# Kernel tuning notes

Measured on AMD Instinct MI355X. Metric: run time of the kernel, lower is better.

Reference implementation:

```python
import jax, jax.numpy as jnp
import numpy as np

N_QUBITS = 16
DIM = 1 << N_QUBITS
NUM_CLASSES = 23
BATCH = 64

# PauliZ sign table: wire 0 is the most-significant bit of the flattened index.
_idx = np.arange(DIM)
SIGNS = np.stack([1 - 2 * ((_idx >> (N_QUBITS - 1 - w)) & 1) for w in range(N_QUBITS)], axis=1).astype(np.float32)  # (DIM, 16)


def _rx_mat(theta):
    c = jnp.cos(theta / 2).astype(jnp.complex64)
    s = (-1j * jnp.sin(theta / 2)).astype(jnp.complex64)
    return jnp.stack([jnp.stack([c, s]), jnp.stack([s, c])])  # (2,2)


def _rot_mat(phi, theta, omega):
    ct = jnp.cos(theta / 2)
    st = jnp.sin(theta / 2)
    a = jnp.exp(-0.5j * (phi + omega)) * ct
    b = -jnp.exp(0.5j * (phi - omega)) * st
    c = jnp.exp(-0.5j * (phi - omega)) * st
    d = jnp.exp(0.5j * (phi + omega)) * ct
    return jnp.stack([jnp.stack([a, b]), jnp.stack([c, d])]).astype(jnp.complex64)


def _apply_1q(state, U, w):
    # state: (B, 2,...,2); shared 2x2 gate on wire w (axis w+1)
    st = jnp.tensordot(state, U, axes=[[w + 1], [1]])  # contracted axis moves to last
    return jnp.moveaxis(st, -1, w + 1)


def _apply_rx_batched(state, theta_b, w):
    # per-sample RX angles theta_b: (B,)
    half = theta_b / 2
    c = jnp.cos(half).astype(jnp.complex64)
    s = (-1j * jnp.sin(half)).astype(jnp.complex64)
    U = jnp.stack([jnp.stack([c, s], -1), jnp.stack([s, c], -1)], -2)  # (B,2,2)
    st = jnp.moveaxis(state, w + 1, -1)
    st = jnp.einsum('bji,b...i->b...j', U, st)
    return jnp.moveaxis(st, -1, w + 1)


def _apply_crx(state, theta, ctrl, tgt):
    s0 = jax.lax.index_in_dim(state, 0, axis=ctrl + 1, keepdims=False)
    s1 = jax.lax.index_in_dim(state, 1, axis=ctrl + 1, keepdims=False)
    tax = tgt + 1 if tgt < ctrl else tgt  # target axis after control axis removal
    U = _rx_mat(theta)
    s1 = jnp.moveaxis(jnp.tensordot(s1, U, axes=[[tax], [1]]), -1, tax)
    return jnp.stack([s0, s1], axis=ctrl + 1)


def _circuit(x, w0, x0, w1, x1):
    B = x.shape[0]
    state = jnp.zeros((B,) + (2,) * N_QUBITS, jnp.complex64)
    state = state.at[(slice(None),) + (0,) * N_QUBITS].set(1.0)
    for w, xc in ((w0, x0), (w1, x1)):
        for q in range(N_QUBITS):
            state = _apply_rx_batched(state, x[:, q], q)
        for q in range(N_QUBITS):
            state = _apply_1q(state, _rot_mat(w[q, 0], w[q, 1], w[q, 2]), q)
        for q in range(N_QUBITS):
            state = _apply_crx(state, xc[q], q, (q + 1) % N_QUBITS)
    probs = (state.real ** 2 + state.imag ** 2).reshape(B, DIM)
    return probs @ jnp.asarray(SIGNS)  # (B, 16) PauliZ expvals


def setup_inputs() -> dict:
    key = jax.random.key(0)
    ks = jax.random.split(key, 7)
    return {
        'x': jax.random.normal(ks[0], (BATCH, N_QUBITS), jnp.float32),
        'w0': jax.random.normal(ks[1], (N_QUBITS, 3), jnp.float32),
        'x0': jax.random.normal(ks[2], (N_QUBITS,), jnp.float32),
        'w1': jax.random.normal(ks[3], (N_QUBITS, 3), jnp.float32),
        'x1': jax.random.normal(ks[4], (N_QUBITS,), jnp.float32),
        'fc_w': jax.random.normal(ks[5], (NUM_CLASSES, N_QUBITS), jnp.float32) * 0.25,
        'fc_b': jax.random.normal(ks[6], (NUM_CLASSES,), jnp.float32) * 0.05,
    }


def reference(x, w0, x0, w1, x1, fc_w, fc_b):
    feats = _circuit(x, w0, x0, w1, x1)           # (B, 16)
    logits = feats @ fc_w.T + fc_b                # (B, 23)
    return jax.nn.log_softmax(logits, axis=1)
```

## Files before the change

kernel.cpp:

```cpp
#include <hip/hip_runtime.h>
#include <hip/hip_bf16.h>


#define DIM 65536
#define BATCH 64
#define PSTR 580


template<int RB>
__device__ __forceinline__ void g1q_reg(float* sr, float* si, const float* U) {
  float u00r=U[0],u00i=U[1],u01r=U[2],u01i=U[3],u10r=U[4],u10i=U[5],u11r=U[6],u11i=U[7];
#pragma unroll
  for (int k = 0; k < 8; ++k) {
    int lo = k & ((1<<RB)-1);
    int j0 = ((k >> RB) << (RB+1)) | lo;
    int j1 = j0 | (1<<RB);
    float a0r=sr[j0], a0i=si[j0], a1r=sr[j1], a1i=si[j1];
    sr[j0] = u00r*a0r - u00i*a0i + u01r*a1r - u01i*a1i;
    si[j0] = u00r*a0i + u00i*a0r + u01r*a1i + u01i*a1r;
    sr[j1] = u10r*a0r - u10i*a0i + u11r*a1r - u11i*a1i;
    si[j1] = u10r*a0i + u10i*a0r + u11r*a1i + u11i*a1r;
  }
}

template<int RB, int CB>
__device__ __forceinline__ void gsel_reg_cc(float* sr, float* si, const float* M0, const float* M1) {
  float a0=M0[0],a1=M0[1],a2=M0[2],a3=M0[3],a4=M0[4],a5=M0[5],a6=M0[6],a7=M0[7];
  float b0=M1[0],b1=M1[1],b2=M1[2],b3=M1[3],b4=M1[4],b5=M1[5],b6=M1[6],b7=M1[7];
#pragma unroll
  for (int k = 0; k < 8; ++k) {
    int lo = k & ((1<<RB)-1);
    int j0 = ((k >> RB) << (RB+1)) | lo;
    int j1 = j0 | (1<<RB);
    const bool c = ((j0 >> CB) & 1) != 0;
    float u00r=c?b0:a0, u00i=c?b1:a1, u01r=c?b2:a2, u01i=c?b3:a3;
    float u10r=c?b4:a4, u10i=c?b5:a5, u11r=c?b6:a6, u11i=c?b7:a7;
    float p0r=sr[j0], p0i=si[j0], p1r=sr[j1], p1i=si[j1];
    sr[j0] = u00r*p0r - u00i*p0i + u01r*p1r - u01i*p1i;
    si[j0] = u00r*p0i + u00i*p0r + u01r*p1i + u01i*p1r;
    sr[j1] = u10r*p0r - u10i*p0i + u11r*p1r - u11i*p1i;
    si[j1] = u10r*p0i + u10i*p0r + u11r*p1i + u11i*p1r;
  }
}

template<int RB>
__device__ __forceinline__ void gsel_reg_pred(float* sr, float* si, const float* M0,
                                              const float* M1, bool ctrl) {
  float u[8];
#pragma unroll
  for (int e = 0; e < 8; ++e) u[e] = ctrl ? M1[e] : M0[e];
  g1q_reg<RB>(sr, si, u);
}

template<int CB, int LB>
__device__ __forceinline__ void crx_reg_lane(float* sr, float* si, float c, float s) {
#pragma unroll
  for (int k = 0; k < 8; ++k) {
    int lo2 = k & ((1<<CB)-1);
    int j = ((((k >> CB) << (CB+1)) | lo2)) | (1<<CB);
    float pr = __shfl_xor(sr[j], 1<<LB, 64);
    float pi = __shfl_xor(si[j], 1<<LB, 64);
    float mr = sr[j], mi = si[j];
    sr[j] = c*mr + s*pi;
    si[j] = c*mi - s*pr;
  }
}

__device__ __forceinline__ int swz(int o) { return o ^ ((o>>4)&15) ^ ((o>>8)&15); }

__device__ __forceinline__ unsigned bfp(float r, float i) {
  unsigned ur = __float_as_uint(r), ui = __float_as_uint(i);
  ur = (ur + 0x7fffu + ((ur >> 16) & 1u)) >> 16;
  ui = (ui + 0x7fffu + ((ui >> 16) & 1u)) & 0xffff0000u;
  return (ur & 0xffffu) | ui;
}
__device__ __forceinline__ float bfr(unsigned u) { return __uint_as_float(u << 16); }
__device__ __forceinline__ float bfi(unsigned u) { return __uint_as_float(u & 0xffff0000u); }

#define MP(Pb, l, q, s) ((Pb) + (((l)*16+(q))*2+(s))*8)


__global__ __launch_bounds__(256) void pB2(unsigned* __restrict__ st,
                                           const float* __restrict__ x, const float* __restrict__ w0,
                                           const float* __restrict__ x0, const float* __restrict__ w1,
                                           const float* __restrict__ x1, float* __restrict__ P,
                                           float* __restrict__ feats, int* __restrict__ ctr) {
  __shared__ float2 lds2[4096];
  __shared__ float Ps[PSTR];
  int blk = blockIdx.x;
  int b = blk >> 4, mp = blk & 15;
  int t = threadIdx.x, lane = t & 63, wv = t >> 6;

  {
    float (*su)[8] = reinterpret_cast<float(*)[8]>(lds2);
    if (mp == 0 && t < 16) feats[b*16 + t] = 0.f;
    if (mp == 0 && t == 16) ctr[b] = 0;
    if (t < 32) {
      int l = t >> 4, q = t & 15;
      const float* W = (l ? w1 : w0) + q*3;
      float xa = 0.5f * x[b*16 + q];
      float cr = cosf(xa), sx = sinf(xa);
      float phi = W[0], th = W[1], om = W[2];
      float ct = cosf(0.5f*th), stt = sinf(0.5f*th);
      float po = 0.5f*(phi+om), pm = 0.5f*(phi-om);
      float ar =  cosf(po)*ct,  ai = -sinf(po)*ct;
      float br = -cosf(pm)*stt, bi = -sinf(pm)*stt;
      float cr2 = cosf(pm)*stt, ci2 = -sinf(pm)*stt;
      float dr =  cosf(po)*ct,  di =  sinf(po)*ct;
      float U[8];
      U[0] = ar*cr + bi*sx;   U[1] = ai*cr - br*sx;
      U[2] = ai*sx + br*cr;   U[3] = -ar*sx + bi*cr;
      U[4] = cr2*cr + di*sx;  U[5] = ci2*cr - dr*sx;
      U[6] = ci2*sx + dr*cr;  U[7] = -cr2*sx + di*cr;
      float* M0 = MP(Ps, l, q, 0);
      float* M1 = M0 + 8;
#pragma unroll
      for (int e = 0; e < 8; ++e) { M0[e] = U[e]; su[t][e] = U[e]; }
      if (q == 0) {
        float ang = l ? 0.5f*x0[15] : 0.f;
        float cg = cosf(ang), sg = sinf(ang);
        M1[0] =  cg*U[0] + sg*U[3];  M1[1] = cg*U[1] - sg*U[2];
        M1[2] =  sg*U[1] + cg*U[2];  M1[3] = -sg*U[0] + cg*U[3];
        M1[4] =  cg*U[4] + sg*U[7];  M1[5] = cg*U[5] - sg*U[6];
        M1[6] =  sg*U[5] + cg*U[6];  M1[7] = -sg*U[4] + cg*U[7];
      } else {
        float ang = 0.5f*(l ? x1[q-1] : x0[q-1]);
        float cg = cosf(ang), sg = sinf(ang);
        M1[0] = cg*U[0] + sg*U[5];  M1[1] = cg*U[1] - sg*U[4];
        M1[2] = cg*U[2] + sg*U[7];  M1[3] = cg*U[3] - sg*U[6];
        M1[4] = cg*U[4] + sg*U[1];  M1[5] = cg*U[5] - sg*U[0];
        M1[6] = cg*U[6] + sg*U[3];  M1[7] = cg*U[7] - sg*U[2];
      }
      if (t == 0) { Ps[576] = cosf(0.5f*x1[15]); Ps[577] = sinf(0.5f*x1[15]); }
    }
    __syncthreads();
  }

  float sr[16], si[16];
#pragma unroll
  for (int r = 0; r < 16; ++r) { sr[r] = 0.f; si[r] = 0.f; }
  if (t == 0) {
    sr[0] = 1.f;
    g1q_reg<3>(sr, si, MP(Ps,0,0,0));
    gsel_reg_cc<2,3>(sr, si, MP(Ps,0,1,0), MP(Ps,0,1,1));
    gsel_reg_cc<1,2>(sr, si, MP(Ps,0,2,0), MP(Ps,0,2,1));
    gsel_reg_cc<0,1>(sr, si, MP(Ps,0,3,0), MP(Ps,0,3,1));
  } else if (t >= 64 && t < 72) {
    float (*su)[8] = reinterpret_cast<float(*)[8]>(lds2);
    int k = t - 64;
    float xr = su[13][((k>>2)&1)*4], xi = su[13][((k>>2)&1)*4+1];
    float yr = su[14][((k>>1)&1)*4], yi = su[14][((k>>1)&1)*4+1];
    float zr = su[15][(k&1)*4],      zi = su[15][(k&1)*4+1];
    float pr = xr*yr - xi*yi, pi = xr*yi + xi*yr;
    float T0r = pr*zr - pi*zi, T0i = pr*zi + pi*zr;
    float a12 = 0.5f*x0[12], c12 = cosf(a12), s12 = sinf(a12);
    float T0r4 = __shfl_xor(T0r, 4, 64), T0i4 = __shfl_xor(T0i, 4, 64);
    float T1r = c12*T0r + s12*T0i4, T1i = c12*T0i - s12*T0r4;
    float a13 = 0.5f*x0[13], c13 = cosf(a13), s13 = sinf(a13);
    float T0r2 = __shfl_xor(T0r, 2, 64), T0i2 = __shfl_xor(T0i, 2, 64);
    float T1r2 = __shfl_xor(T1r, 2, 64), T1i2 = __shfl_xor(T1i, 2, 64);
    float n0r, n0i, n1r, n1i;
    if (k & 4) {
      n0r = c13*T0r + s13*T0i2; n0i = c13*T0i - s13*T0r2;
      n1r = c13*T1r + s13*T1i2; n1i = c13*T1i - s13*T1r2;
    } else { n0r = T0r; n0i = T0i; n1r = T1r; n1i = T1i; }
    float a14 = 0.5f*x0[14], c14 = cosf(a14), s14 = sinf(a14);
    float n0r1 = __shfl_xor(n0r, 1, 64), n0i1 = __shfl_xor(n0i, 1, 64);
    float n1r1 = __shfl_xor(n1r, 1, 64), n1i1 = __shfl_xor(n1i, 1, 64);
    float F0r, F0i, F1r, F1i;
    if (k & 2) {
      F0r = c14*n0r + s14*n0i1; F0i = c14*n0i - s14*n0r1;
      F1r = c14*n1r + s14*n1i1; F1i = c14*n1i - s14*n1r1;
    } else { F0r = n0r; F0i = n0i; F1r = n1r; F1i = n1i; }
    const float* A = MP(Ps,0,12,0);
    const float* B = MP(Ps,0,12,1);
    float* T2 = Ps + 512;
#pragma unroll
    for (int j0 = 0; j0 < 2; ++j0) {
      float tr = j0 ? F1r : F0r, ti = j0 ? F1i : F0i;
#pragma unroll
      for (int j1 = 0; j1 < 2; ++j1) {
        const float* Wm = j1 ? B : A;
        float fr = Wm[j0*4], fi = Wm[j0*4+1];
        T2[((j0*2 + j1)*8 + k)*2 + 0] = tr*fr - ti*fi;
        T2[((j0*2 + j1)*8 + k)*2 + 1] = tr*fi + ti*fr;
      }
    }
  }
  if (mp == 0) {
    if (t >= 192) P[(size_t)b*PSTR + 256 + t] = Ps[256 + t];
    else if (t == 1) { P[(size_t)b*PSTR + 576] = Ps[576]; P[(size_t)b*PSTR + 577] = Ps[577]; }
  }
  __syncthreads();

#pragma unroll
  for (int r = 0; r < 16; ++r) {
    int o = wv | (lane << 2) | (r << 8);
    lds2[swz(o)] = make_float2(sr[r], si[r]);
  }
  __syncthreads();
#pragma unroll
  for (int r = 0; r < 16; ++r) {
    int o = wv | (((lane>>4)&3) << 2) | (r << 4) | ((lane&15) << 8);
    float2 v = lds2[swz(o)]; sr[r] = v.x; si[r] = v.y;
  }
  if (t < 16) {
    gsel_reg_pred<3>(sr, si, MP(Ps,0,4,0), MP(Ps,0,4,1), (lane&1)!=0);
    gsel_reg_cc<2,3>(sr, si, MP(Ps,0,5,0), MP(Ps,0,5,1));
    gsel_reg_cc<1,2>(sr, si, MP(Ps,0,6,0), MP(Ps,0,6,1));
    gsel_reg_cc<0,1>(sr, si, MP(Ps,0,7,0), MP(Ps,0,7,1));
  }
#pragma unroll
  for (int r = 0; r < 16; ++r) {
    int o = wv | (((lane>>4)&3) << 2) | (r << 4) | ((lane&15) << 8);
    lds2[swz(o)] = make_float2(sr[r], si[r]);
  }
  __syncthreads();
#pragma unroll
  for (int r = 0; r < 16; ++r) {
    int o = r | (lane << 4) | (wv << 10);
    float2 v = lds2[swz(o)]; sr[r] = v.x; si[r] = v.y;
  }
  gsel_reg_pred<3>(sr, si, MP(Ps,0,8,0), MP(Ps,0,8,1), (lane&1)!=0);
  gsel_reg_cc<2,3>(sr, si, MP(Ps,0,9,0), MP(Ps,0,9,1));
  gsel_reg_cc<1,2>(sr, si, MP(Ps,0,10,0), MP(Ps,0,10,1));
  gsel_reg_cc<0,1>(sr, si, MP(Ps,0,11,0), MP(Ps,0,11,1));
  __syncthreads();
#pragma unroll
  for (int r = 0; r < 16; ++r) {
    int paddr = ((lane>>4)&3) | (wv << 2) | (r << 4) | ((lane&15) << 8);
    lds2[swz(paddr)] = make_float2(sr[r], si[r]);
  }
  __syncthreads();

  {
#pragma unroll
    for (int r = 0; r < 16; ++r) {
      int paddr = r | (lane << 4) | (wv << 10);
      float2 v = lds2[swz(paddr)]; sr[r] = v.x; si[r] = v.y;
    }
    int k = mp & 7;
    const float* tf = Ps + 512 + (((((mp>>3)&1)*2 + (lane&1))*8 + k)*2);
    float fr = tf[0], fi = tf[1];
    const float* M = (mp&1) ? MP(Ps,1,0,1) : MP(Ps,1,0,0);
    float v8[8];
#pragma unroll
    for (int e = 0; e < 4; ++e) {
      v8[2*e]   = fr*M[2*e]   - fi*M[2*e+1];
      v8[2*e+1] = fr*M[2*e+1] + fi*M[2*e];
    }
    g1q_reg<3>(sr, si, v8);
  }
  gsel_reg_cc<2,3>(sr, si, MP(Ps,1,1,0), MP(Ps,1,1,1));
  gsel_reg_cc<1,2>(sr, si, MP(Ps,1,2,0), MP(Ps,1,2,1));
  gsel_reg_cc<0,1>(sr, si, MP(Ps,1,3,0), MP(Ps,1,3,1));
  __syncthreads();
#pragma unroll
  for (int r = 0; r < 16; ++r) {
    int o = lane | (wv << 6) | (r << 8);
    lds2[swz(o)] = make_float2(sr[r], si[r]);
  }
  __syncthreads();
#pragma unroll
  for (int r = 0; r < 16; ++r) {
    int o = wv | (((lane>>4)&3) << 2) | (r << 4) | ((lane&15) << 8);
    float2 v = lds2[swz(o)]; sr[r] = v.x; si[r] = v.y;
  }
  gsel_reg_pred<3>(sr, si, MP(Ps,1,4,0), MP(Ps,1,4,1), (lane&1)!=0);
  gsel_reg_cc<2,3>(sr, si, MP(Ps,1,5,0), MP(Ps,1,5,1));
  gsel_reg_cc<1,2>(sr, si, MP(Ps,1,6,0), MP(Ps,1,6,1));
  gsel_reg_cc<0,1>(sr, si, MP(Ps,1,7,0), MP(Ps,1,7,1));
#pragma unroll
  for (int r = 0; r < 16; ++r) {
    int o = wv | (((lane>>4)&3) << 2) | (r << 4) | ((lane&15) << 8);
    lds2[swz(o)] = make_float2(sr[r], si[r]);
  }
  __syncthreads();
#pragma unroll
  for (int r = 0; r < 16; ++r) {
    int o = r | (lane << 4) | (wv << 10);
    float2 v = lds2[swz(o)]; sr[r] = v.x; si[r] = v.y;
  }
  gsel_reg_pred<3>(sr, si, MP(Ps,1,8,0), MP(Ps,1,8,1), (lane&1)!=0);
  gsel_reg_cc<2,3>(sr, si, MP(Ps,1,9,0), MP(Ps,1,9,1));
  gsel_reg_cc<1,2>(sr, si, MP(Ps,1,10,0), MP(Ps,1,10,1));
  gsel_reg_cc<0,1>(sr, si, MP(Ps,1,11,0), MP(Ps,1,11,1));
  {
    int sbase = (lane << 4) | (wv << 10) | (mp << 12);
    uint4* dst = (uint4*)(st + (size_t)b*DIM + sbase);
#pragma unroll
    for (int g = 0; g < 4; ++g)
      dst[g] = make_uint4(bfp(sr[4*g],si[4*g]), bfp(sr[4*g+1],si[4*g+1]),
                          bfp(sr[4*g+2],si[4*g+2]), bfp(sr[4*g+3],si[4*g+3]));
  }
}


__global__ __launch_bounds__(512) void p3(const unsigned* __restrict__ st, const float* __restrict__ P,
                                          float* __restrict__ feats, int* __restrict__ ctr,
                                          const float* __restrict__ fcw, const float* __restrict__ fcb,
                                          float* __restrict__ out) {
  int blk = blockIdx.x;
  int b = blk >> 3, n = blk & 7;
  int t = threadIdx.x, lane = t & 63, wv = t >> 6;
  const float* Pb = P + (size_t)b*PSTR;
  int base = (lane&31) | (wv << 5) | (n << 8) | ((lane>>5) << 11);
  const unsigned* S = st + (size_t)b*DIM + base;
  float sr[16], si[16];
#pragma unroll
  for (int r = 0; r < 16; ++r) { unsigned u = S[r << 12]; sr[r] = bfr(u); si[r] = bfi(u); }

  gsel_reg_pred<3>(sr, si, MP(Pb,1,12,0), MP(Pb,1,12,1), (lane&1)!=0);
  gsel_reg_cc<2,3>(sr, si, MP(Pb,1,13,0), MP(Pb,1,13,1));
  gsel_reg_cc<1,2>(sr, si, MP(Pb,1,14,0), MP(Pb,1,14,1));
  gsel_reg_cc<0,1>(sr, si, MP(Pb,1,15,0), MP(Pb,1,15,1));
  crx_reg_lane<0,5>(sr, si, Pb[576], Pb[577]);

  float tot=0.f, sA=0.f, sB=0.f, sC=0.f, sD=0.f;
#pragma unroll
  for (int r = 0; r < 16; ++r) {
    float p = sr[r]*sr[r] + si[r]*si[r];
    tot += p;
    sA += (r & 1) ? -p : p;
    sB += (r & 2) ? -p : p;
    sC += (r & 4) ? -p : p;
    sD += (r & 8) ? -p : p;
  }
  float f[16];
  f[15] = sA; f[14] = sB; f[13] = sC; f[12] = sD;
  f[11] = (lane&1)  ? -tot : tot;
  f[10] = (lane&2)  ? -tot : tot;
  f[9]  = (lane&4)  ? -tot : tot;
  f[8]  = (lane&8)  ? -tot : tot;
  f[7]  = (lane&16) ? -tot : tot;
  f[0]  = (lane&32) ? -tot : tot;
  f[6]  = (wv&1)    ? -tot : tot;
  f[5]  = (wv&2)    ? -tot : tot;
  f[4]  = (wv&4)    ? -tot : tot;
  f[3]  = (n&1)     ? -tot : tot;
  f[2]  = (n&2)     ? -tot : tot;
  f[1]  = (n&4)     ? -tot : tot;
#pragma unroll
  for (int w = 0; w < 16; ++w) {
#pragma unroll
    for (int off = 32; off; off >>= 1) f[w] += __shfl_xor(f[w], off, 64);
  }
  __shared__ float red[8][17];
  if (lane == 0) {
#pragma unroll
    for (int w = 0; w < 16; ++w) red[wv][w] = f[w];
  }
  __syncthreads();
  if (t < 16) {
    float acc = 0.f;
#pragma unroll
    for (int i = 0; i < 8; ++i) acc += red[i][t];
    atomicAdd(&feats[b*16 + t], acc);
  }

  __shared__ int flagS;
  __syncthreads();
  if (t == 0) { __threadfence(); flagS = atomicAdd(&ctr[b], 1); }
  __syncthreads();
  if (flagS == 7) {
    __shared__ float fs[16];
    __shared__ float lg[23];
    if (t < 16) fs[t] = __hip_atomic_load(&feats[b*16 + t], __ATOMIC_RELAXED, __HIP_MEMORY_SCOPE_AGENT);
    __syncthreads();
    if (t < 23) {
      float acc = fcb[t];
#pragma unroll
      for (int w = 0; w < 16; ++w) acc += fs[w] * fcw[t*16 + w];
      lg[t] = acc;
    }
    __syncthreads();
    if (t < 23) {
      float mx = -1e30f;
#pragma unroll
      for (int j = 0; j < 23; ++j) mx = fmaxf(mx, lg[j]);
      float Ssum = 0.f;
#pragma unroll
      for (int j = 0; j < 23; ++j) Ssum += expf(lg[j] - mx);
      out[b*23 + t] = lg[t] - mx - logf(Ssum);
    }
  }
}

extern "C" void kernel_launch(void* const* d_in, const int* in_sizes, int n_in,
                              void* d_out, int out_size, void* d_ws, size_t ws_size,
                              hipStream_t stream) {
  const float* x   = (const float*)d_in[0];
  const float* w0  = (const float*)d_in[1];
  const float* x0  = (const float*)d_in[2];
  const float* w1  = (const float*)d_in[3];
  const float* x1  = (const float*)d_in[4];
  const float* fcw = (const float*)d_in[5];
  const float* fcb = (const float*)d_in[6];
  float* out = (float*)d_out;

  char* ws = (char*)d_ws;
  unsigned* st  = (unsigned*)ws;
  float*  P     = (float*)(ws + (size_t)BATCH * DIM * 4);
  float*  feats = P + (size_t)BATCH * PSTR;
  int*    ctr   = (int*)(feats + BATCH*16);

  pB2<<<1024, 256, 0, stream>>>(st, x, w0, x0, w1, x1, P, feats, ctr);
  p3<<<512, 512, 0, stream>>>(st, P, feats, ctr, fcw, fcb, out);
  (void)in_sizes; (void)n_in; (void)out_size; (void)ws_size;
}
```

Baseline: 125.1 us.

## Fuse final gate and readout kernel into first kernel via per-sample spin barrier

Merges the second kernel into the first. The 16 blocks of each batch sample meet at a global atomic counter spin-wait, then read back the bf16 state and apply the last gates, the measurement and the log-softmax. Gate parameters stay in LDS, so the P buffer round-trip and the second launch go away. In exchange it adds a hipMemsetAsync and a grid-wide spin barrier. That barrier can deadlock unless all 16 blocks of a sample are co-resident, and the readout now uses 256-thread blocks instead of 512.

Measured after the change: 388.3 us. 3.1x slower.

```diff
diff --git a/kernel.cpp b/kernel.cpp
--- a/kernel.cpp
+++ b/kernel.cpp
@@ -80,21 +80,22 @@
 #define MP(Pb, l, q, s) ((Pb) + (((l)*16+(q))*2+(s))*8)
 
 
-__global__ __launch_bounds__(256) void pB2(unsigned* __restrict__ st,
+__global__ __launch_bounds__(256) void pF2(unsigned* __restrict__ st,
                                            const float* __restrict__ x, const float* __restrict__ w0,
                                            const float* __restrict__ x0, const float* __restrict__ w1,
-                                           const float* __restrict__ x1, float* __restrict__ P,
-                                           float* __restrict__ feats, int* __restrict__ ctr) {
+                                           const float* __restrict__ x1,
+                                           const float* __restrict__ fcw, const float* __restrict__ fcb,
+                                           float* __restrict__ out, float* __restrict__ feats,
+                                           int* __restrict__ ctr, int* __restrict__ ctr2) {
   __shared__ float2 lds2[4096];
   __shared__ float Ps[PSTR];
+  __shared__ int flagS2;
   int blk = blockIdx.x;
   int b = blk >> 4, mp = blk & 15;
   int t = threadIdx.x, lane = t & 63, wv = t >> 6;
 
   {
     float (*su)[8] = reinterpret_cast<float(*)[8]>(lds2);
-    if (mp == 0 && t < 16) feats[b*16 + t] = 0.f;
-    if (mp == 0 && t == 16) ctr[b] = 0;
     if (t < 32) {
       int l = t >> 4, q = t & 15;
       const float* W = (l ? w1 : w0) + q*3;
@@ -187,10 +188,6 @@
       }
     }
   }
-  if (mp == 0) {
-    if (t >= 192) P[(size_t)b*PSTR + 256 + t] = Ps[256 + t];
-    else if (t == 1) { P[(size_t)b*PSTR + 576] = Ps[576]; P[(size_t)b*PSTR + 577] = Ps[577]; }
-  }
   __syncthreads();
 
 #pragma unroll
@@ -293,95 +290,95 @@
       dst[g] = make_uint4(bfp(sr[4*g],si[4*g]), bfp(sr[4*g+1],si[4*g+1]),
                           bfp(sr[4*g+2],si[4*g+2]), bfp(sr[4*g+3],si[4*g+3]));
   }
-}
-
-
-__global__ __launch_bounds__(512) void p3(const unsigned* __restrict__ st, const float* __restrict__ P,
-                                          float* __restrict__ feats, int* __restrict__ ctr,
-                                          const float* __restrict__ fcw, const float* __restrict__ fcb,
-                                          float* __restrict__ out) {
-  int blk = blockIdx.x;
-  int b = blk >> 3, n = blk & 7;
-  int t = threadIdx.x, lane = t & 63, wv = t >> 6;
-  const float* Pb = P + (size_t)b*PSTR;
-  int base = (lane&31) | (wv << 5) | (n << 8) | ((lane>>5) << 11);
-  const unsigned* S = st + (size_t)b*DIM + base;
-  float sr[16], si[16];
-#pragma unroll
-  for (int r = 0; r < 16; ++r) { unsigned u = S[r << 12]; sr[r] = bfr(u); si[r] = bfi(u); }
-
-  gsel_reg_pred<3>(sr, si, MP(Pb,1,12,0), MP(Pb,1,12,1), (lane&1)!=0);
-  gsel_reg_cc<2,3>(sr, si, MP(Pb,1,13,0), MP(Pb,1,13,1));
-  gsel_reg_cc<1,2>(sr, si, MP(Pb,1,14,0), MP(Pb,1,14,1));
-  gsel_reg_cc<0,1>(sr, si, MP(Pb,1,15,0), MP(Pb,1,15,1));
-  crx_reg_lane<0,5>(sr, si, Pb[576], Pb[577]);
-
-  float tot=0.f, sA=0.f, sB=0.f, sC=0.f, sD=0.f;
-#pragma unroll
-  for (int r = 0; r < 16; ++r) {
-    float p = sr[r]*sr[r] + si[r]*si[r];
-    tot += p;
-    sA += (r & 1) ? -p : p;
-    sB += (r & 2) ? -p : p;
-    sC += (r & 4) ? -p : p;
-    sD += (r & 8) ? -p : p;
-  }
-  float f[16];
-  f[15] = sA; f[14] = sB; f[13] = sC; f[12] = sD;
-  f[11] = (lane&1)  ? -tot : tot;
-  f[10] = (lane&2)  ? -tot : tot;
-  f[9]  = (lane&4)  ? -tot : tot;
-  f[8]  = (lane&8)  ? -tot : tot;
-  f[7]  = (lane&16) ? -tot : tot;
-  f[0]  = (lane&32) ? -tot : tot;
-  f[6]  = (wv&1)    ? -tot : tot;
-  f[5]  = (wv&2)    ? -tot : tot;
-  f[4]  = (wv&4)    ? -tot : tot;
-  f[3]  = (n&1)     ? -tot : tot;
-  f[2]  = (n&2)     ? -tot : tot;
-  f[1]  = (n&4)     ? -tot : tot;
-#pragma unroll
-  for (int w = 0; w < 16; ++w) {
-#pragma unroll
-    for (int off = 32; off; off >>= 1) f[w] += __shfl_xor(f[w], off, 64);
-  }
-  __shared__ float red[8][17];
-  if (lane == 0) {
-#pragma unroll
-    for (int w = 0; w < 16; ++w) red[wv][w] = f[w];
-  }
-  __syncthreads();
-  if (t < 16) {
-    float acc = 0.f;
-#pragma unroll
-    for (int i = 0; i < 8; ++i) acc += red[i][t];
-    atomicAdd(&feats[b*16 + t], acc);
-  }
-
-  __shared__ int flagS;
-  __syncthreads();
-  if (t == 0) { __threadfence(); flagS = atomicAdd(&ctr[b], 1); }
-  __syncthreads();
-  if (flagS == 7) {
-    __shared__ float fs[16];
-    __shared__ float lg[23];
-    if (t < 16) fs[t] = __hip_atomic_load(&feats[b*16 + t], __ATOMIC_RELAXED, __HIP_MEMORY_SCOPE_AGENT);
+
+  __threadfence();
+  __syncthreads();
+  if (t == 0) {
+    atomicAdd(&ctr[b], 1);
+    while (__hip_atomic_load(&ctr[b], __ATOMIC_ACQUIRE, __HIP_MEMORY_SCOPE_AGENT) < 16)
+      __builtin_amdgcn_s_sleep(4);
+  }
+  __syncthreads();
+  __threadfence();
+
+  {
+    int base = (lane&31) | (wv << 5) | (((mp>>3)&1) << 7) | ((mp&7) << 8) | ((lane>>5) << 11);
+    const unsigned* S = st + (size_t)b*DIM + base;
+#pragma unroll
+    for (int r = 0; r < 16; ++r) { unsigned u = S[r << 12]; sr[r] = bfr(u); si[r] = bfi(u); }
+
+    gsel_reg_pred<3>(sr, si, MP(Ps,1,12,0), MP(Ps,1,12,1), (lane&1)!=0);
+    gsel_reg_cc<2,3>(sr, si, MP(Ps,1,13,0), MP(Ps,1,13,1));
+    gsel_reg_cc<1,2>(sr, si, MP(Ps,1,14,0), MP(Ps,1,14,1));
+    gsel_reg_cc<0,1>(sr, si, MP(Ps,1,15,0), MP(Ps,1,15,1));
+    crx_reg_lane<0,5>(sr, si, Ps[576], Ps[577]);
+
+    float tot=0.f, sA=0.f, sB=0.f, sC=0.f, sD=0.f;
+#pragma unroll
+    for (int r = 0; r < 16; ++r) {
+      float p = sr[r]*sr[r] + si[r]*si[r];
+      tot += p;
+      sA += (r & 1) ? -p : p;
+      sB += (r & 2) ? -p : p;
+      sC += (r & 4) ? -p : p;
+      sD += (r & 8) ? -p : p;
+    }
+    float f[16];
+    f[15] = sA; f[14] = sB; f[13] = sC; f[12] = sD;
+    f[11] = (lane&1)  ? -tot : tot;
+    f[10] = (lane&2)  ? -tot : tot;
+    f[9]  = (lane&4)  ? -tot : tot;
+    f[8]  = (lane&8)  ? -tot : tot;
+    f[7]  = (lane&16) ? -tot : tot;
+    f[0]  = (lane&32) ? -tot : tot;
+    f[6]  = (wv&1)    ? -tot : tot;
+    f[5]  = (wv&2)    ? -tot : tot;
+    f[4]  = (mp&8)    ? -tot : tot;
+    f[3]  = (mp&1)    ? -tot : tot;
+    f[2]  = (mp&2)    ? -tot : tot;
+    f[1]  = (mp&4)    ? -tot : tot;
+#pragma unroll
+    for (int w = 0; w < 16; ++w) {
+#pragma unroll
+      for (int off = 32; off; off >>= 1) f[w] += __shfl_xor(f[w], off, 64);
+    }
+    float* shm = (float*)lds2;
+    if (lane == 0) {
+#pragma unroll
+      for (int w = 0; w < 16; ++w) shm[wv*17 + w] = f[w];
+    }
     __syncthreads();
-    if (t < 23) {
-      float acc = fcb[t];
-#pragma unroll
-      for (int w = 0; w < 16; ++w) acc += fs[w] * fcw[t*16 + w];
-      lg[t] = acc;
-    }
+    if (t < 16) {
+      float acc = 0.f;
+#pragma unroll
+      for (int i = 0; i < 4; ++i) acc += shm[i*17 + t];
+      atomicAdd(&feats[b*16 + t], acc);
+    }
+
     __syncthreads();
-    if (t < 23) {
-      float mx = -1e30f;
-#pragma unroll
-      for (int j = 0; j < 23; ++j) mx = fmaxf(mx, lg[j]);
-      float Ssum = 0.f;
-#pragma unroll
-      for (int j = 0; j < 23; ++j) Ssum += expf(lg[j] - mx);
-      out[b*23 + t] = lg[t] - mx - logf(Ssum);
+    if (t == 0) { __threadfence(); flagS2 = atomicAdd(&ctr2[b], 1); }
+    __syncthreads();
+    if (flagS2 == 15) {
+      float* fs = shm + 96;
+      float* lg = shm + 128;
+      if (t < 16) fs[t] = __hip_atomic_load(&feats[b*16 + t], __ATOMIC_RELAXED, __HIP_MEMORY_SCOPE_AGENT);
+      __syncthreads();
+      if (t < 23) {
+        float acc = fcb[t];
+#pragma unroll
+        for (int w = 0; w < 16; ++w) acc += fs[w] * fcw[t*16 + w];
+        lg[t] = acc;
+      }
+      __syncthreads();
+      if (t < 23) {
+        float mx = -1e30f;
+#pragma unroll
+        for (int j = 0; j < 23; ++j) mx = fmaxf(mx, lg[j]);
+        float Ssum = 0.f;
+#pragma unroll
+        for (int j = 0; j < 23; ++j) Ssum += expf(lg[j] - mx);
+        out[b*23 + t] = lg[t] - mx - logf(Ssum);
+      }
     }
   }
 }
@@ -400,11 +397,11 @@
 
   char* ws = (char*)d_ws;
   unsigned* st  = (unsigned*)ws;
-  float*  P     = (float*)(ws + (size_t)BATCH * DIM * 4);
-  float*  feats = P + (size_t)BATCH * PSTR;
+  float*  feats = (float*)(ws + (size_t)BATCH * DIM * 4);
   int*    ctr   = (int*)(feats + BATCH*16);
-
-  pB2<<<1024, 256, 0, stream>>>(st, x, w0, x0, w1, x1, P, feats, ctr);
-  p3<<<512, 512, 0, stream>>>(st, P, feats, ctr, fcw, fcb, out);
+  int*    ctr2  = ctr + BATCH;
+
+  hipMemsetAsync(feats, 0, BATCH*16*sizeof(float) + 2*BATCH*sizeof(int), stream);
+  pF2<<<1024, 256, 0, stream>>>(st, x, w0, x0, w1, x1, fcw, fcb, out, feats, ctr, ctr2);
   (void)in_sizes; (void)n_in; (void)out_size; (void)ws_size;
 }
```
